# Kernel optimization log

Measured on AMD Instinct MI355X. Metric: run time of the kernel, lower is better.

## Reference

```python
import jax, jax.numpy as jnp
import numpy as np
from jax import lax

B, C, H, W = 4, 128, 128, 128   # batch, norm_nc, spatial
L = 19                           # label_nc / number of style components
S = 512                          # style_length == nhidden
EPS = 1e-5


def _conv5(x, w, b):
    # 5x5 'SAME' conv, NCHW / OIHW
    y = lax.conv_general_dilated(x, w, (1, 1), 'SAME',
                                 dimension_numbers=('NCHW', 'OIHW', 'NCHW'))
    return y + b[None, :, None, None]


def _instance_norm(x):
    mu = jnp.mean(x, axis=(2, 3), keepdims=True)
    var = jnp.var(x, axis=(2, 3), keepdims=True)
    return (x - mu) * lax.rsqrt(var + EPS)


def setup_inputs() -> dict:
    key = jax.random.key(0)
    ks = jax.random.split(key, 16)
    x = jax.random.normal(ks[0], (B, C, H, W), dtype=jnp.float32)
    seg_ids = jax.random.randint(ks[1], (B, H, W), 0, L)
    segmap = jax.nn.one_hot(seg_ids, L, dtype=jnp.float32).transpose(0, 3, 1, 2)  # [B,L,H,W]
    style_codes = jax.random.normal(ks[2], (B, L, S), dtype=jnp.float32)
    sc = 0.02
    fc_w = jax.random.normal(ks[3], (L, S, S), dtype=jnp.float32) * sc  # [j, out, in]
    fc_b = jnp.zeros((L, S), dtype=jnp.float32)
    conv_gamma_w = jax.random.normal(ks[4], (C, S, 5, 5), dtype=jnp.float32) * sc
    conv_gamma_b = jnp.zeros((C,), dtype=jnp.float32)
    conv_beta_w = jax.random.normal(ks[5], (C, S, 5, 5), dtype=jnp.float32) * sc
    conv_beta_b = jnp.zeros((C,), dtype=jnp.float32)
    spade_shared_w = jax.random.normal(ks[6], (S, L, 5, 5), dtype=jnp.float32) * sc
    spade_shared_b = jnp.zeros((S,), dtype=jnp.float32)
    spade_gamma_w = jax.random.normal(ks[7], (C, S, 5, 5), dtype=jnp.float32) * sc
    spade_gamma_b = jnp.zeros((C,), dtype=jnp.float32)
    spade_beta_w = jax.random.normal(ks[8], (C, S, 5, 5), dtype=jnp.float32) * sc
    spade_beta_b = jnp.zeros((C,), dtype=jnp.float32)
    blending_gamma = jnp.zeros((1,), dtype=jnp.float32)
    blending_beta = jnp.zeros((1,), dtype=jnp.float32)
    return dict(x=x, segmap=segmap, style_codes=style_codes,
                fc_w=fc_w, fc_b=fc_b,
                conv_gamma_w=conv_gamma_w, conv_gamma_b=conv_gamma_b,
                conv_beta_w=conv_beta_w, conv_beta_b=conv_beta_b,
                spade_shared_w=spade_shared_w, spade_shared_b=spade_shared_b,
                spade_gamma_w=spade_gamma_w, spade_gamma_b=spade_gamma_b,
                spade_beta_w=spade_beta_w, spade_beta_b=spade_beta_b,
                blending_gamma=blending_gamma, blending_beta=blending_beta)


def reference(x, segmap, style_codes, fc_w, fc_b,
              conv_gamma_w, conv_gamma_b, conv_beta_w, conv_beta_b,
              spade_shared_w, spade_shared_b, spade_gamma_w, spade_gamma_b,
              spade_beta_w, spade_beta_b, blending_gamma, blending_beta):
    normalized = _instance_norm(x)
    # segmap already at x's spatial size -> nearest interpolate is identity.
    # Batched per-component Linear + ReLU: mu[b,j,:] = relu(style_codes[b,j] @ fc_w[j].T + fc_b[j])
    mu = jax.nn.relu(jnp.einsum('bjd,jed->bje', style_codes, fc_w) + fc_b)  # [B,L,S]
    # Vectorized equivalent of the per-region masked_scatter_ (segmap channels disjoint one-hot):
    middle_avg = jnp.einsum('bjhw,bje->behw', segmap, mu)  # [B,S,H,W]
    gamma_avg = _conv5(middle_avg, conv_gamma_w, conv_gamma_b)
    beta_avg = _conv5(middle_avg, conv_beta_w, conv_beta_b)
    actv = jax.nn.relu(_conv5(segmap, spade_shared_w, spade_shared_b))
    gamma_spade = _conv5(actv, spade_gamma_w, spade_gamma_b)
    beta_spade = _conv5(actv, spade_beta_w, spade_beta_b)
    ga = jax.nn.sigmoid(blending_gamma)[0]
    ba = jax.nn.sigmoid(blending_beta)[0]
    gamma_final = ga * gamma_avg + (1 - ga) * gamma_spade
    beta_final = ba * beta_avg + (1 - ba) * beta_spade
    return normalized * (1 + gamma_final) + beta_final
```

## Files before the change

### kernel.cpp

```cpp
#include <hip/hip_runtime.h>
#include <stdint.h>

#define BB 4
#define CC 128
#define HH 128
#define WW 128
#define LL 19
#define SS 512
#define HP 132
#define NPIX (HH*WW)
#define PCELLS (HP*HP)
#define NCELL (BB*PCELLS)

#define SA 192.0f
#define SW 1024.0f
#define INVQ (1.0f/(SA*SW))
#define INVSW (1.0f/SW)

typedef float f32x4 __attribute__((ext_vector_type(4)));
typedef int   i32x4 __attribute__((ext_vector_type(4)));
typedef short s16x8 __attribute__((ext_vector_type(8)));

#define AS1Q __attribute__((address_space(1)))
#define AS3Q __attribute__((address_space(3)))
#define MEMFENCE asm volatile("" ::: "memory")

__device__ __forceinline__ void gld16(const void* g, void* l){
  __builtin_amdgcn_global_load_lds((const AS1Q void*)g, (AS3Q void*)l, 16, 0, 0);
}

__device__ inline unsigned short f2bf(float v){
  unsigned u = __float_as_uint(v);
  return (unsigned short)((u + 0x7fffu + ((u >> 16) & 1u)) >> 16);
}
__device__ inline float bflo(unsigned u){ return __uint_as_float(u << 16); }
__device__ inline float bfhi(unsigned u){ return __uint_as_float(u & 0xffff0000u); }

__global__ __launch_bounds__(256) void k_pre(
                      const float* __restrict__ x, float* __restrict__ mean,
                      float* __restrict__ rstd,
                      const float* __restrict__ seg, int* __restrict__ ids,
                      const float* __restrict__ style, const float* __restrict__ fcw,
                      const float* __restrict__ fcb, float* __restrict__ mu,
                      const float* __restrict__ cgw, const float* __restrict__ cbw,
                      float* __restrict__ Wtg, float* __restrict__ Wtb,
                      const float* __restrict__ ssw, short* __restrict__ Tt16,
                      const float* __restrict__ sgw, const float* __restrict__ sbw,
                      unsigned* __restrict__ W2q){
  __shared__ float shmem[12800];
  const int blk = blockIdx.x;
  const int t = threadIdx.x;
  if (blk < 512){
    const int bc = blk;
    const int w = t >> 6, lane = t & 63;
    const float4* xv = (const float4*)(x + (size_t)bc * NPIX);
    float s = 0.f, q = 0.f;
    for (int i = t; i < NPIX/4; i += 256){
      float4 v = xv[i];
      s += v.x + v.y + v.z + v.w;
      q += v.x*v.x + v.y*v.y + v.z*v.z + v.w*v.w;
    }
    #pragma unroll
    for (int off = 32; off; off >>= 1){ s += __shfl_down(s, off); q += __shfl_down(q, off); }
    if (lane == 0){ shmem[w] = s; shmem[4 + w] = q; }
    __syncthreads();
    if (t == 0){
      float S = shmem[0]+shmem[1]+shmem[2]+shmem[3];
      float Q = shmem[4]+shmem[5]+shmem[6]+shmem[7];
      float mn = S * (1.f/16384.f);
      float var = Q * (1.f/16384.f) - mn*mn;
      mean[bc] = mn;
      rstd[bc] = rsqrtf(var + 1e-5f);
    }
  } else if (blk < 785){
    int idx = (blk - 512)*256 + t;
    if (idx >= NCELL) return;
    int b = idx / PCELLS; int rem = idx - b*PCELLS;
    int r = rem / HP;     int cp = rem - r*HP;
    int id = LL;
    if (r >= 2 && r <= 129 && cp >= 2 && cp <= 129){
      int p = (r-2)*WW + (cp-2);
      const float* sp = seg + (size_t)b*LL*NPIX + p;
      id = 0;
      for (int j = 0; j < LL; ++j){
        if (sp[(size_t)j*NPIX] > 0.5f){ id = j; break; }
      }
    }
    ids[idx] = id;
  } else if (blk < 861){
    const int jb = blk - 785;
    const int j = jb >> 2, part = jb & 3;
    const int w = t >> 6, lane = t & 63;
    float (*s_s)[SS] = (float(*)[SS])shmem;
    for (int i = t; i < 4*SS; i += 256){
      int b = i >> 9, e = i & 511;
      s_s[b][e] = style[(size_t)(b*LL + j)*SS + e];
    }
    __syncthreads();
    for (int e = part*128 + w; e < part*128 + 128; e += 4){
      const float* row = fcw + ((size_t)(j*SS + e))*SS;
      float a0=0.f, a1=0.f, a2=0.f, a3=0.f;
      #pragma unroll
      for (int i = 0; i < 8; ++i){
        int d = lane + i*64; float rv = row[d];
        a0 += s_s[0][d]*rv; a1 += s_s[1][d]*rv;
        a2 += s_s[2][d]*rv; a3 += s_s[3][d]*rv;
      }
      #pragma unroll
      for (int off = 32; off; off >>= 1){
        a0 += __shfl_down(a0,off); a1 += __shfl_down(a1,off);
        a2 += __shfl_down(a2,off); a3 += __shfl_down(a3,off);
      }
      if (lane == 0){
        float fb = fcb[j*SS + e];
        mu[(size_t)(0*LL+j)*SS + e] = fmaxf(a0+fb, 0.f);
        mu[(size_t)(1*LL+j)*SS + e] = fmaxf(a1+fb, 0.f);
        mu[(size_t)(2*LL+j)*SS + e] = fmaxf(a2+fb, 0.f);
        mu[(size_t)(3*LL+j)*SS + e] = fmaxf(a3+fb, 0.f);
      }
    }
  } else if (blk < 1117){
    int pb = blk - 861;
    int c = pb >> 1;
    const float* src = ((pb & 1) ? cbw : cgw) + (size_t)c*12800;
    float* dst = ((pb & 1) ? Wtb : Wtg) + (size_t)c*12800;
    for (int i = t; i < 12800; i += 256) shmem[i] = src[i];
    __syncthreads();
    for (int i = t; i < 12800; i += 256){
      int dd = i >> 9, e = i & 511;
      dst[i] = shmem[e*25 + dd];
    }
  } else if (blk < 2117){
    int idx = (blk-1117)*256 + t;
    int s = idx & 511; int rest = idx >> 9;
    int j = rest / 25, d = rest - (rest/25)*25;
    float v = 0.f;
    if (j < LL) v = ssw[((size_t)s*LL + j)*25 + d];
    int q = (int)rintf(v * SW);
    q = q > 32767 ? 32767 : (q < -32768 ? -32768 : q);
    Tt16[idx] = (short)q;
  } else {
    int cpr = blk - 2117;
    const float* w = (cpr < 128) ? sgw : sbw;
    int c = cpr & 127;
    const float* src = w + (size_t)c*12800;
    for (int i = t; i < 12800; i += 256) shmem[i] = src[i];
    __syncthreads();
    for (int wd = t; wd < 3200; wd += 256){
      int r4 = wd*4; int tt = r4 >> 6; int k0 = r4 & 63;
      int schunk = tt/25, tap = tt - schunk*25;
      unsigned pack = 0;
      #pragma unroll
      for (int i = 0; i < 4; ++i){
        int s = schunk*64 + k0 + i;
        int q = (int)rintf(shmem[s*25 + tap] * SW);
        q = q > 127 ? 127 : (q < -127 ? -127 : q);
        pack |= ((unsigned)(q & 0xFF)) << (8*i);
      }
      W2q[(size_t)cpr*3200 + wd] = pack;
    }
  }
}

__global__ void k_gtab(const float* __restrict__ mu, const float* __restrict__ Wtg,
                       const float* __restrict__ Wtb, float2* __restrict__ G){
  const int blk = blockIdx.x;
  const int b = blk >> 7, c = blk & 127;
  const int t = threadIdx.x, w = t >> 6, lane = t & 63;
  __shared__ float mu_s[LL*SS];
  for (int i = t; i < LL*SS; i += 256) mu_s[i] = mu[(size_t)b*LL*SS + i];
  __syncthreads();
  for (int i = 0; i < 125; ++i){
    int o = i*4 + w;
    int j = o / 25, d = o - (o/25)*25;
    float ag = 0.f, ab = 0.f;
    if (j < LL){
      const float4* wg4 = (const float4*)(Wtg + ((size_t)c*25 + d)*SS);
      const float4* wb4 = (const float4*)(Wtb + ((size_t)c*25 + d)*SS);
      const float4* m4p = (const float4*)(mu_s + j*SS);
      #pragma unroll
      for (int rp = 0; rp < 2; ++rp){
        int e4 = rp*64 + lane;
        float4 m4 = m4p[e4];
        float4 wv = wg4[e4];
        ag += m4.x*wv.x + m4.y*wv.y + m4.z*wv.z + m4.w*wv.w;
        float4 wv2 = wb4[e4];
        ab += m4.x*wv2.x + m4.y*wv2.y + m4.z*wv2.z + m4.w*wv2.w;
      }
      #pragma unroll
      for (int off = 32; off; off >>= 1){ ag += __shfl_down(ag, off); ab += __shfl_down(ab, off); }
    }
    if (lane == 0) G[((size_t)(b*CC + c))*500 + o] = make_float2(ag, ab);
  }
}

__global__ __launch_bounds__(512) void k_actv(
    const int* __restrict__ ids, const short* __restrict__ Tt16,
    const float* __restrict__ ssb, uint2* __restrict__ actv8){
  __shared__ short Tl[500*72];
  const int t = threadIdx.x, w = t >> 6, lane = t & 63;
  const int cs  = blockIdx.x & 7;
  const int cg0 = blockIdx.x >> 3;
  for (int i = t; i < 4000; i += 512){
    int row = i >> 3, sub = i & 7;
    int4 v = *(const int4*)(Tt16 + (size_t)row*512 + cs*64 + sub*8);
    *(int4*)(Tl + row*72 + sub*8) = v;
  }
  __syncthreads();
  const int chsub = lane & 7;
  const int csub  = lane >> 3;
  float bias[8];
  #pragma unroll
  for (int i = 0; i < 8; ++i) bias[i] = ssb[cs*64 + chsub*8 + i];
  for (int it = 0; it < 4; ++it){
    int cell = cg0*256 + it*64 + w*8 + csub;
    if (cell >= NCELL) break;
    int b = cell / PCELLS; int rem = cell - b*PCELLS;
    int r = rem / HP;      int cp = rem - r*HP;
    uint2 outv = {0u, 0u};
    if (r >= 2 && r <= 129 && cp >= 2 && cp <= 129){
      const int* idb = ids + b*PCELLS + (r-2)*HP + (cp-2);
      s16x8 acc = {0,0,0,0,0,0,0,0};
      #pragma unroll
      for (int dy = 0; dy < 5; ++dy){
        const int* row5 = idb + dy*HP;
        #pragma unroll
        for (int dx = 0; dx < 5; ++dx){
          int id = row5[dx];
          acc += *(const s16x8*)(Tl + (id*25 + dy*5 + dx)*72 + chsub*8);
        }
      }
      unsigned q[8];
      #pragma unroll
      for (int i = 0; i < 8; ++i){
        float a = (float)acc[i] * INVSW + bias[i];
        int v = (int)(fmaxf(a, 0.f)*SA + 0.5f);
        q[i] = (unsigned)(v > 127 ? 127 : v);
      }
      outv.x = q[0] | (q[1]<<8) | (q[2]<<16) | (q[3]<<24);
      outv.y = q[4] | (q[5]<<8) | (q[6]<<16) | (q[7]<<24);
    }
    actv8[(size_t)cell*64 + cs*8 + chsub] = outv;
  }
}

__global__ __launch_bounds__(512, 2) void k_conv(
    const unsigned char* __restrict__ actv8,
    const unsigned char* __restrict__ W2q,
    unsigned short* __restrict__ spade)
{
  __shared__ int4 lds4[131072/16];
  char* ldsb = (char*)lds4;
  const int bid = blockIdx.x;
  const int blk = (bid & 7)*32 + (bid >> 3);
  const int b  = blk >> 6;
  const int y0 = (blk & 63) * 2;
  const int t  = threadIdx.x;
  const int lane = t & 63;
  const int w  = t >> 6;
  const int wr = w >> 2, wc = w & 3;
  const int li = lane & 15, q = lane >> 4;

  const int lsub  = lane >> 2;
  const int s_src = (lane & 3) ^ ((lane >> 3) & 3);
  const bool isA  = (w < 4);
  const char* p0[4];
  int ldsrel[4];
  #pragma unroll
  for (int l = 0; l < 4; ++l){
    int row = (isA ? w : (w - 4)) * 64 + l*16 + lsub;
    if (isA){
      int y = y0 + (row >> 7), x = row & 127;
      p0[l] = (const char*)(actv8 + (((size_t)b*HP + y)*HP + x)*SS + s_src*16);
    } else {
      p0[l] = (const char*)(W2q + (size_t)row*12800 + s_src*16);
    }
    ldsrel[l] = w*4096 + l*1024 + lane*16;
  }

  auto stage_tt = [&](int tt){
    int schunk = tt / 25; int tap = tt - schunk*25;
    int dy = tap / 5, dx = tap - dy*5;
    size_t offA = (size_t)(dy*HP + dx)*SS + (size_t)schunk*64;
    size_t off = isA ? offA : (size_t)tt * 64;
    char* base = ldsb + ((tt & 3) * 32768);
    #pragma unroll
    for (int l = 0; l < 4; ++l)
      gld16(p0[l] + off, base + ldsrel[l]);
  };

  i32x4 acc[8][4];
  #pragma unroll
  for (int m = 0; m < 8; ++m)
    #pragma unroll
    for (int n = 0; n < 4; ++n) acc[m][n] = (i32x4){0,0,0,0};

  const int swz  = (q ^ ((li >> 1) & 3)) * 16;
  const int arel = (wr*128 + li)*64 + swz;
  const int brel = 16384 + (wc*64 + li)*64 + swz;

  i32x4 a03[2][4], bv[2][4], a47[4];

  stage_tt(0); stage_tt(1); stage_tt(2);
  asm volatile("s_waitcnt vmcnt(8)" ::: "memory");
  __builtin_amdgcn_s_barrier();
  MEMFENCE;
  #pragma unroll
  for (int m = 0; m < 4; ++m) a03[0][m] = *(const i32x4*)(ldsb + arel + m*1024);
  #pragma unroll
  for (int n = 0; n < 4; ++n) bv[0][n]  = *(const i32x4*)(ldsb + brel + n*1024);

  for (int T2 = 0; T2 < 99; ++T2){
    #pragma unroll
    for (int half = 0; half < 2; ++half){
      const int T = 2*T2 + half;
      const char* buf  = ldsb + ((unsigned)T & 3u)*32768;
      const char* bufn = ldsb + ((unsigned)(T+1) & 3u)*32768;
      const int cur = half, nxt = half ^ 1;
      #pragma unroll
      for (int m = 0; m < 4; ++m) a47[m] = *(const i32x4*)(buf + arel + (m+4)*1024);
      MEMFENCE;
      asm volatile("s_waitcnt vmcnt(4)" ::: "memory");
      __builtin_amdgcn_s_barrier();
      MEMFENCE;
      if (T <= 196) stage_tt(T + 3);
      MEMFENCE;
      __builtin_amdgcn_s_setprio(1);
      #pragma unroll
      for (int m = 0; m < 4; ++m)
        #pragma unroll
        for (int n = 0; n < 4; ++n)
          acc[m][n] = __builtin_amdgcn_mfma_i32_16x16x64_i8(a03[cur][m], bv[cur][n], acc[m][n], 0, 0, 0);
      __builtin_amdgcn_s_setprio(0);
      MEMFENCE;
      #pragma unroll
      for (int m = 0; m < 4; ++m) a03[nxt][m] = *(const i32x4*)(bufn + arel + m*1024);
      #pragma unroll
      for (int n = 0; n < 4; ++n) bv[nxt][n]  = *(const i32x4*)(bufn + brel + n*1024);
      MEMFENCE;
      __builtin_amdgcn_s_setprio(1);
      #pragma unroll
      for (int m = 0; m < 4; ++m)
        #pragma unroll
        for (int n = 0; n < 4; ++n)
          acc[m+4][n] = __builtin_amdgcn_mfma_i32_16x16x64_i8(a47[m], bv[cur][n], acc[m+4][n], 0, 0, 0);
      __builtin_amdgcn_s_setprio(0);
      MEMFENCE;
    }
  }
  {
    const char* buf  = ldsb + (198 & 3)*32768;
    const char* bufn = ldsb + (199 & 3)*32768;
    #pragma unroll
    for (int m = 0; m < 4; ++m) a47[m] = *(const i32x4*)(buf + arel + (m+4)*1024);
    MEMFENCE;
    asm volatile("s_waitcnt vmcnt(0)" ::: "memory");
    __builtin_amdgcn_s_barrier();
    MEMFENCE;
    #pragma unroll
    for (int m = 0; m < 4; ++m)
      #pragma unroll
      for (int n = 0; n < 4; ++n)
        acc[m][n] = __builtin_amdgcn_mfma_i32_16x16x64_i8(a03[0][m], bv[0][n], acc[m][n], 0, 0, 0);
    #pragma unroll
    for (int m = 0; m < 4; ++m) a03[1][m] = *(const i32x4*)(bufn + arel + m*1024);
    #pragma unroll
    for (int n = 0; n < 4; ++n) bv[1][n]  = *(const i32x4*)(bufn + brel + n*1024);
    #pragma unroll
    for (int m = 0; m < 4; ++m)
      #pragma unroll
      for (int n = 0; n < 4; ++n)
        acc[m+4][n] = __builtin_amdgcn_mfma_i32_16x16x64_i8(a47[m], bv[0][n], acc[m+4][n], 0, 0, 0);
  }
  {
    const char* buf = ldsb + (199 & 3)*32768;
    #pragma unroll
    for (int m = 0; m < 4; ++m) a47[m] = *(const i32x4*)(buf + arel + (m+4)*1024);
    #pragma unroll
    for (int m = 0; m < 4; ++m)
      #pragma unroll
      for (int n = 0; n < 4; ++n)
        acc[m][n] = __builtin_amdgcn_mfma_i32_16x16x64_i8(a03[1][m], bv[1][n], acc[m][n], 0, 0, 0);
    #pragma unroll
    for (int m = 0; m < 4; ++m)
      #pragma unroll
      for (int n = 0; n < 4; ++n)
        acc[m+4][n] = __builtin_amdgcn_mfma_i32_16x16x64_i8(a47[m], bv[1][n], acc[m+4][n], 0, 0, 0);
  }

  const int xq4 = (lane >> 4) << 2;
  const int cq  = wc*64 + (lane & 15);
  #pragma unroll
  for (int m = 0; m < 8; ++m){
    int p = wr*128 + m*16 + xq4;
    int y = y0 + (p >> 7), x = p & 127;
    #pragma unroll
    for (int n = 0; n < 4; ++n){
      int cp = cq + n*16;
      i32x4 a = acc[m][n];
      uint2 pk;
      pk.x = (unsigned)f2bf((float)a.x * INVQ) | ((unsigned)f2bf((float)a.y * INVQ) << 16);
      pk.y = (unsigned)f2bf((float)a.z * INVQ) | ((unsigned)f2bf((float)a.w * INVQ) << 16);
      *(uint2*)(spade + (((size_t)(b*256 + cp))*HH + y)*WW + x) = pk;
    }
  }
}

__global__ void k_final(const float* __restrict__ xin, const int* __restrict__ ids,
                        const float2* __restrict__ G, const unsigned short* __restrict__ spade,
                        const float* __restrict__ mean, const float* __restrict__ rstd,
                        const float* __restrict__ cgb, const float* __restrict__ cbb,
                        const float* __restrict__ sgb, const float* __restrict__ sbb,
                        const float* __restrict__ bgam, const float* __restrict__ bbet,
                        float* __restrict__ out){
  const int blk = blockIdx.x;
  const int b = blk >> 7, c = blk & 127;
  const int t = threadIdx.x;
  __shared__ float2 Gl2[500];
  for (int i = t; i < 500; i += 256){
    int j = i / 25, d = i - (i/25)*25;
    Gl2[d*20 + j] = G[((size_t)(b*CC + c))*500 + i];
  }
  __syncthreads();
  const float ga = 1.f/(1.f + __expf(-bgam[0]));
  const float ba = 1.f/(1.f + __expf(-bbet[0]));
  const float mn = mean[b*CC + c], rs = rstd[b*CC + c];
  const float cg = cgb[c], cb = cbb[c], sg = sgb[c], sb = sbb[c];
  const float* xp  = xin + (size_t)(b*CC + c)*NPIX;
  const unsigned short* spg = spade + (size_t)(b*256 + c)*NPIX;
  const unsigned short* spb = spade + (size_t)(b*256 + c + 128)*NPIX;
  float* op = out + (size_t)(b*CC + c)*NPIX;
  const int* idb = ids + b*PCELLS;
  for (int p2 = t; p2 < NPIX/2; p2 += 256){
    int p = p2*2;
    int y = p >> 7, x = p & 127;
    float ag0=0.f, ab0=0.f, ag1=0.f, ab1=0.f;
    #pragma unroll
    for (int dy = 0; dy < 5; ++dy){
      const int* row = idb + (y+dy)*HP + x;
      int2 v01 = *(const int2*)(row);
      int2 v23 = *(const int2*)(row + 2);
      int2 v45 = *(const int2*)(row + 4);
      int idv[6] = {v01.x, v01.y, v23.x, v23.y, v45.x, v45.y};
      #pragma unroll
      for (int dx = 0; dx < 5; ++dx){
        float2 g0 = Gl2[(dy*5+dx)*20 + idv[dx]];
        float2 g1 = Gl2[(dy*5+dx)*20 + idv[dx+1]];
        ag0 += g0.x; ab0 += g0.y;
        ag1 += g1.x; ab1 += g1.y;
      }
    }
    unsigned sg2 = *(const unsigned*)(spg + p);
    unsigned sb2 = *(const unsigned*)(spb + p);
    float2 xv = *(const float2*)(xp + p);
    float gf0 = ga*(ag0 + cg) + (1.f - ga)*(bflo(sg2) + sg);
    float bf0 = ba*(ab0 + cb) + (1.f - ba)*(bflo(sb2) + sb);
    float gf1 = ga*(ag1 + cg) + (1.f - ga)*(bfhi(sg2) + sg);
    float bf1 = ba*(ab1 + cb) + (1.f - ba)*(bfhi(sb2) + sb);
    float2 ov;
    ov.x = (xv.x - mn)*rs*(1.f + gf0) + bf0;
    ov.y = (xv.y - mn)*rs*(1.f + gf1) + bf1;
    *(float2*)(op + p) = ov;
  }
}

extern "C" void kernel_launch(void* const* d_in, const int* in_sizes, int n_in,
                              void* d_out, int out_size, void* d_ws, size_t ws_size,
                              hipStream_t stream){
  const float* x    = (const float*)d_in[0];
  const float* seg  = (const float*)d_in[1];
  const float* sty  = (const float*)d_in[2];
  const float* fcw  = (const float*)d_in[3];
  const float* fcb  = (const float*)d_in[4];
  const float* cgw  = (const float*)d_in[5];
  const float* cgb  = (const float*)d_in[6];
  const float* cbw  = (const float*)d_in[7];
  const float* cbb  = (const float*)d_in[8];
  const float* ssw  = (const float*)d_in[9];
  const float* ssb  = (const float*)d_in[10];
  const float* sgw  = (const float*)d_in[11];
  const float* sgb  = (const float*)d_in[12];
  const float* sbw  = (const float*)d_in[13];
  const float* sbb  = (const float*)d_in[14];
  const float* bgam = (const float*)d_in[15];
  const float* bbet = (const float*)d_in[16];
  float* out = (float*)d_out;

  char* ws = (char*)d_ws;
  size_t o = 0;
  auto alloc = [&](size_t n){ size_t r = o; o = (o + n + 255) & ~(size_t)255; return r; };
  float* mean          = (float*)(ws + alloc(512*4));
  float* rstd          = (float*)(ws + alloc(512*4));
  int*   ids           = (int*)  (ws + alloc((size_t)NCELL*4));
  float* mu            = (float*)(ws + alloc((size_t)BB*LL*SS*4));
  float2* G            = (float2*)(ws + alloc((size_t)BB*CC*500*8));
  short* Tt16          = (short*)(ws + alloc((size_t)20*25*SS*2));
  unsigned char* W2q   = (unsigned char*)(ws + alloc((size_t)256*12800));
  unsigned char* actv8 = (unsigned char*)(ws + alloc((size_t)NCELL*SS));
  unsigned short* spade= (unsigned short*)(ws + alloc((size_t)BB*256*NPIX*2 < (size_t)2*128*25*512*4
                                                      ? (size_t)2*128*25*512*4
                                                      : (size_t)BB*256*NPIX*2));
  float* Wtg = (float*)spade;
  float* Wtb = (float*)spade + (size_t)128*25*512;
  (void)o; (void)ws_size; (void)in_sizes; (void)n_in; (void)out_size; (void)sty;

  k_pre  <<<dim3(2373), dim3(256), 0, stream>>>(x, mean, rstd, seg, ids,
                                                sty, fcw, fcb, mu,
                                                cgw, cbw, Wtg, Wtb,
                                                ssw, Tt16, sgw, sbw, (unsigned*)W2q);
  k_gtab <<<dim3(512),  dim3(256), 0, stream>>>(mu, Wtg, Wtb, G);
  k_actv <<<dim3(2184), dim3(512), 0, stream>>>(ids, Tt16, ssb, (uint2*)actv8);
  k_conv <<<dim3(256),  dim3(512), 0, stream>>>(actv8, W2q, spade);
  k_final<<<dim3(512),  dim3(256), 0, stream>>>(x, ids, G, spade, mean, rstd,
                                                cgb, cbb, sgb, sbb, bgam, bbet, out);
}
```

Baseline: 365.1 us.

## Merge gtab and actv kernels, store conv weights as bf16, drop fences

```diff
diff --git a/kernel.cpp b/kernel.cpp
--- a/kernel.cpp
+++ b/kernel.cpp
@@ -43,7 +43,7 @@
                       const float* __restrict__ style, const float* __restrict__ fcw,
                       const float* __restrict__ fcb, float* __restrict__ mu,
                       const float* __restrict__ cgw, const float* __restrict__ cbw,
-                      float* __restrict__ Wtg, float* __restrict__ Wtb,
+                      unsigned short* __restrict__ Wtg16, unsigned short* __restrict__ Wtb16,
                       const float* __restrict__ ssw, short* __restrict__ Tt16,
                       const float* __restrict__ sgw, const float* __restrict__ sbw,
                       unsigned* __restrict__ W2q){
@@ -123,12 +123,12 @@
     int pb = blk - 861;
     int c = pb >> 1;
     const float* src = ((pb & 1) ? cbw : cgw) + (size_t)c*12800;
-    float* dst = ((pb & 1) ? Wtb : Wtg) + (size_t)c*12800;
+    unsigned short* dst = ((pb & 1) ? Wtb16 : Wtg16) + (size_t)c*12800;
     for (int i = t; i < 12800; i += 256) shmem[i] = src[i];
     __syncthreads();
     for (int i = t; i < 12800; i += 256){
       int dd = i >> 9, e = i & 511;
-      dst[i] = shmem[e*25 + dd];
+      dst[i] = f2bf(shmem[e*25 + dd]);
     }
   } else if (blk < 2117){
     int idx = (blk-1117)*256 + t;
@@ -162,85 +162,85 @@
   }
 }
 
-__global__ void k_gtab(const float* __restrict__ mu, const float* __restrict__ Wtg,
-                       const float* __restrict__ Wtb, float2* __restrict__ G){
-  const int blk = blockIdx.x;
-  const int b = blk >> 7, c = blk & 127;
-  const int t = threadIdx.x, w = t >> 6, lane = t & 63;
-  __shared__ float mu_s[LL*SS];
-  for (int i = t; i < LL*SS; i += 256) mu_s[i] = mu[(size_t)b*LL*SS + i];
-  __syncthreads();
-  for (int i = 0; i < 125; ++i){
-    int o = i*4 + w;
-    int j = o / 25, d = o - (o/25)*25;
-    float ag = 0.f, ab = 0.f;
-    if (j < LL){
-      const float4* wg4 = (const float4*)(Wtg + ((size_t)c*25 + d)*SS);
-      const float4* wb4 = (const float4*)(Wtb + ((size_t)c*25 + d)*SS);
-      const float4* m4p = (const float4*)(mu_s + j*SS);
-      #pragma unroll
-      for (int rp = 0; rp < 2; ++rp){
-        int e4 = rp*64 + lane;
-        float4 m4 = m4p[e4];
-        float4 wv = wg4[e4];
-        ag += m4.x*wv.x + m4.y*wv.y + m4.z*wv.z + m4.w*wv.w;
-        float4 wv2 = wb4[e4];
-        ab += m4.x*wv2.x + m4.y*wv2.y + m4.z*wv2.z + m4.w*wv2.w;
-      }
-      #pragma unroll
-      for (int off = 32; off; off >>= 1){ ag += __shfl_down(ag, off); ab += __shfl_down(ab, off); }
-    }
-    if (lane == 0) G[((size_t)(b*CC + c))*500 + o] = make_float2(ag, ab);
-  }
-}
-
-__global__ __launch_bounds__(512) void k_actv(
+__global__ __launch_bounds__(512) void k_mid(
+    const float* __restrict__ mu, const unsigned short* __restrict__ Wtg16,
+    const unsigned short* __restrict__ Wtb16, float2* __restrict__ G,
     const int* __restrict__ ids, const short* __restrict__ Tt16,
     const float* __restrict__ ssb, uint2* __restrict__ actv8){
-  __shared__ short Tl[500*72];
+  __shared__ char smem[72000];
+  const int blk = blockIdx.x;
   const int t = threadIdx.x, w = t >> 6, lane = t & 63;
-  const int cs  = blockIdx.x & 7;
-  const int cg0 = blockIdx.x >> 3;
-  for (int i = t; i < 4000; i += 512){
-    int row = i >> 3, sub = i & 7;
-    int4 v = *(const int4*)(Tt16 + (size_t)row*512 + cs*64 + sub*8);
-    *(int4*)(Tl + row*72 + sub*8) = v;
-  }
-  __syncthreads();
-  const int chsub = lane & 7;
-  const int csub  = lane >> 3;
-  float bias[8];
-  #pragma unroll
-  for (int i = 0; i < 8; ++i) bias[i] = ssb[cs*64 + chsub*8 + i];
-  for (int it = 0; it < 4; ++it){
-    int cell = cg0*256 + it*64 + w*8 + csub;
-    if (cell >= NCELL) break;
-    int b = cell / PCELLS; int rem = cell - b*PCELLS;
-    int r = rem / HP;      int cp = rem - r*HP;
-    uint2 outv = {0u, 0u};
-    if (r >= 2 && r <= 129 && cp >= 2 && cp <= 129){
-      const int* idb = ids + b*PCELLS + (r-2)*HP + (cp-2);
-      s16x8 acc = {0,0,0,0,0,0,0,0};
-      #pragma unroll
-      for (int dy = 0; dy < 5; ++dy){
-        const int* row5 = idb + dy*HP;
+  if (blk < 512){
+    float* mu_s = (float*)smem;
+    const int b = blk >> 7, c = blk & 127;
+    for (int i = t; i < LL*SS; i += 512) mu_s[i] = mu[(size_t)b*LL*SS + i];
+    __syncthreads();
+    for (int i = 0; i < 63; ++i){
+      int o = i*8 + w;
+      if (o >= 500) break;
+      int j = o / 25, d = o - (o/25)*25;
+      float ag = 0.f, ab = 0.f;
+      if (j < LL){
+        uint4 wg = *(const uint4*)(Wtg16 + ((size_t)c*25 + d)*SS + lane*8);
+        uint4 wb = *(const uint4*)(Wtb16 + ((size_t)c*25 + d)*SS + lane*8);
+        const float* mp = mu_s + j*SS + lane*8;
+        float4 m0 = *(const float4*)mp;
+        float4 m1 = *(const float4*)(mp + 4);
+        ag = m0.x*bflo(wg.x) + m0.y*bfhi(wg.x) + m0.z*bflo(wg.y) + m0.w*bfhi(wg.y)
+           + m1.x*bflo(wg.z) + m1.y*bfhi(wg.z) + m1.z*bflo(wg.w) + m1.w*bfhi(wg.w);
+        ab = m0.x*bflo(wb.x) + m0.y*bfhi(wb.x) + m0.z*bflo(wb.y) + m0.w*bfhi(wb.y)
+           + m1.x*bflo(wb.z) + m1.y*bfhi(wb.z) + m1.z*bflo(wb.w) + m1.w*bfhi(wb.w);
+      }
+      #pragma unroll
+      for (int off = 32; off; off >>= 1){ ag += __shfl_down(ag, off); ab += __shfl_down(ab, off); }
+      if (lane == 0) G[((size_t)(b*CC + c))*500 + o] = make_float2(ag, ab);
+    }
+  } else {
+    short* Tl = (short*)smem;
+    const int ab2 = blk - 512;
+    const int cs  = ab2 & 7;
+    const int cg0 = ab2 >> 3;
+    for (int i = t; i < 4000; i += 512){
+      int row = i >> 3, sub = i & 7;
+      int4 v = *(const int4*)(Tt16 + (size_t)row*512 + cs*64 + sub*8);
+      *(int4*)(Tl + row*72 + sub*8) = v;
+    }
+    __syncthreads();
+    const int chsub = lane & 7;
+    const int csub  = lane >> 3;
+    float bias[8];
+    #pragma unroll
+    for (int i = 0; i < 8; ++i) bias[i] = ssb[cs*64 + chsub*8 + i];
+    for (int it = 0; it < 4; ++it){
+      int cell = cg0*256 + it*64 + w*8 + csub;
+      if (cell >= NCELL) break;
+      int b = cell / PCELLS; int rem = cell - b*PCELLS;
+      int r = rem / HP;      int cp = rem - r*HP;
+      uint2 outv = {0u, 0u};
+      if (r >= 2 && r <= 129 && cp >= 2 && cp <= 129){
+        const int* idb = ids + b*PCELLS + (r-2)*HP + (cp-2);
+        s16x8 acc = {0,0,0,0,0,0,0,0};
         #pragma unroll
-        for (int dx = 0; dx < 5; ++dx){
-          int id = row5[dx];
-          acc += *(const s16x8*)(Tl + (id*25 + dy*5 + dx)*72 + chsub*8);
+        for (int dy = 0; dy < 5; ++dy){
+          const int* row5 = idb + dy*HP;
+          #pragma unroll
+          for (int dx = 0; dx < 5; ++dx){
+            int id = row5[dx];
+            acc += *(const s16x8*)(Tl + (id*25 + dy*5 + dx)*72 + chsub*8);
+          }
         }
-      }
-      unsigned q[8];
-      #pragma unroll
-      for (int i = 0; i < 8; ++i){
-        float a = (float)acc[i] * INVSW + bias[i];
-        int v = (int)(fmaxf(a, 0.f)*SA + 0.5f);
-        q[i] = (unsigned)(v > 127 ? 127 : v);
-      }
-      outv.x = q[0] | (q[1]<<8) | (q[2]<<16) | (q[3]<<24);
-      outv.y = q[4] | (q[5]<<8) | (q[6]<<16) | (q[7]<<24);
-    }
-    actv8[(size_t)cell*64 + cs*8 + chsub] = outv;
+        unsigned q[8];
+        #pragma unroll
+        for (int i = 0; i < 8; ++i){
+          float a = (float)acc[i] * INVSW + bias[i];
+          int v = (int)(fmaxf(a, 0.f)*SA + 0.5f);
+          q[i] = (unsigned)(v > 127 ? 127 : v);
+        }
+        outv.x = q[0] | (q[1]<<8) | (q[2]<<16) | (q[3]<<24);
+        outv.y = q[4] | (q[5]<<8) | (q[6]<<16) | (q[7]<<24);
+      }
+      actv8[(size_t)cell*64 + cs*8 + chsub] = outv;
+    }
   }
 }
 
@@ -332,12 +332,10 @@
         for (int n = 0; n < 4; ++n)
           acc[m][n] = __builtin_amdgcn_mfma_i32_16x16x64_i8(a03[cur][m], bv[cur][n], acc[m][n], 0, 0, 0);
       __builtin_amdgcn_s_setprio(0);
-      MEMFENCE;
       #pragma unroll
       for (int m = 0; m < 4; ++m) a03[nxt][m] = *(const i32x4*)(bufn + arel + m*1024);
       #pragma unroll
       for (int n = 0; n < 4; ++n) bv[nxt][n]  = *(const i32x4*)(bufn + brel + n*1024);
-      MEMFENCE;
       __builtin_amdgcn_s_setprio(1);
       #pragma unroll
       for (int m = 0; m < 4; ++m)
@@ -497,19 +495,17 @@
   short* Tt16          = (short*)(ws + alloc((size_t)20*25*SS*2));
   unsigned char* W2q   = (unsigned char*)(ws + alloc((size_t)256*12800));
   unsigned char* actv8 = (unsigned char*)(ws + alloc((size_t)NCELL*SS));
-  unsigned short* spade= (unsigned short*)(ws + alloc((size_t)BB*256*NPIX*2 < (size_t)2*128*25*512*4
-                                                      ? (size_t)2*128*25*512*4
-                                                      : (size_t)BB*256*NPIX*2));
-  float* Wtg = (float*)spade;
-  float* Wtb = (float*)spade + (size_t)128*25*512;
+  unsigned short* spade= (unsigned short*)(ws + alloc((size_t)BB*256*NPIX*2));
+  unsigned short* Wtg16 = spade;
+  unsigned short* Wtb16 = spade + (size_t)128*25*512;
   (void)o; (void)ws_size; (void)in_sizes; (void)n_in; (void)out_size; (void)sty;
 
   k_pre  <<<dim3(2373), dim3(256), 0, stream>>>(x, mean, rstd, seg, ids,
                                                 sty, fcw, fcb, mu,
-                                                cgw, cbw, Wtg, Wtb,
+                                                cgw, cbw, Wtg16, Wtb16,
                                                 ssw, Tt16, sgw, sbw, (unsigned*)W2q);
-  k_gtab <<<dim3(512),  dim3(256), 0, stream>>>(mu, Wtg, Wtb, G);
-  k_actv <<<dim3(2184), dim3(512), 0, stream>>>(ids, Tt16, ssb, (uint2*)actv8);
+  k_mid  <<<dim3(2696), dim3(512), 0, stream>>>(mu, Wtg16, Wtb16, G,
+                                                ids, Tt16, ssb, (uint2*)actv8);
   k_conv <<<dim3(256),  dim3(512), 0, stream>>>(actv8, W2q, spade);
   k_final<<<dim3(512),  dim3(256), 0, stream>>>(x, ids, G, spade, mean, rstd,
                                                 cgb, cbb, sgb, sbb, bgam, bbet, out);
```

After: 343.0 us. 6.0% less time.
